# Kernel optimization log

Measured on AMD Instinct MI355X. Metric: run time of the kernel, lower is better.

## Reference

```python
import jax, jax.numpy as jnp
import numpy as np

NUM_USERS = 100000
NUM_ITEMS = 50000
EMBED_DIM = 64
N_NODES = NUM_USERS + NUM_ITEMS
N_EDGES = 4800000
N_LAYERS = 3


def setup_inputs() -> dict:
    key = jax.random.key(0)
    k = jax.random.split(key, 7)
    return {
        "users": jax.random.randint(k[0], (16384,), 0, NUM_USERS),
        "items": jax.random.randint(k[1], (16384,), 0, NUM_ITEMS),
        "user_emb": jax.random.normal(k[2], (NUM_USERS, EMBED_DIM), dtype=jnp.float32) * 0.1,
        "item_emb": jax.random.normal(k[3], (NUM_ITEMS, EMBED_DIM), dtype=jnp.float32) * 0.1,
        "adj_rows": jax.random.randint(k[4], (N_EDGES,), 0, N_NODES),
        "adj_cols": jax.random.randint(k[5], (N_EDGES,), 0, N_NODES),
        "adj_vals": jax.random.uniform(k[6], (N_EDGES,), dtype=jnp.float32) * (1.0 / 32.0),
    }


def _spmm(rows, cols, vals, x):
    # y[r] = sum_{e: rows[e]==r} vals[e] * x[cols[e]]   (COO SpMM)
    msgs = vals[:, None] * x[cols]              # [nnz, d]
    return jax.ops.segment_sum(msgs, rows, num_segments=N_NODES)


def reference(users, items, user_emb, item_emb, adj_rows, adj_cols, adj_vals):
    ego = jnp.concatenate([user_emb, item_emb], axis=0)   # [N, d]
    acc = ego                                             # running sum of layer outputs
    h = ego
    for _ in range(N_LAYERS):
        h = _spmm(adj_rows, adj_cols, adj_vals, h)
        acc = acc + h
    final = acc / jnp.asarray(N_LAYERS + 1, dtype=acc.dtype)  # mean over layers
    final_users = final[:NUM_USERS]
    final_items = final[NUM_USERS:]
    u = final_users[users]                                # [B, d]
    v = final_items[items]                                # [B, d]
    return jnp.sum(u * v, axis=1)                         # [B]
```

## Files before the change

kernel.cpp:

```cpp
#include <hip/hip_runtime.h>

#define NUM_USERS 100000
#define NUM_ITEMS 50000
#define EMBED_DIM 64
#define N_NODES   (NUM_USERS + NUM_ITEMS)
#define N_EDGES   4800000
#define N_QUERY   16384

#define NODE_FLOATS ((size_t)N_NODES * EMBED_DIM)
#define NODE_FLOAT4 (NODE_FLOATS / 4)

#define NBUCKET    256
#define BROWS      586
#define BUCKET_CAP 20480
#define BIN_EDGES  8192
#define BIN_THREADS 512
#define BIN_BLOCKS ((N_EDGES + BIN_EDGES - 1) / BIN_EDGES)

__device__ __forceinline__ float4 bf2f4(uint2 u) {
    float4 f;
    f.x = __uint_as_float(u.x << 16);
    f.y = __uint_as_float(u.x & 0xFFFF0000u);
    f.z = __uint_as_float(u.y << 16);
    f.w = __uint_as_float(u.y & 0xFFFF0000u);
    return f;
}
__device__ __forceinline__ unsigned rne_bf(float f) {
    unsigned b = __float_as_uint(f);
    return (b + 0x7FFFu + ((b >> 16) & 1u)) >> 16;
}
__device__ __forceinline__ uint2 f42bf(float4 f) {
    uint2 u;
    u.x = rne_bf(f.x) | (rne_bf(f.y) << 16);
    u.y = rne_bf(f.z) | (rne_bf(f.w) << 16);
    return u;
}
__device__ __forceinline__ void fma4v(float v, float4 xv, float4& av) {
    av.x = fmaf(v, xv.x, av.x);
    av.y = fmaf(v, xv.y, av.y);
    av.z = fmaf(v, xv.z, av.z);
    av.w = fmaf(v, xv.w, av.w);
}

__global__ void init_gcur_kernel(int* __restrict__ gcur) {
    if (threadIdx.x < NBUCKET)
        gcur[threadIdx.x] = threadIdx.x * BUCKET_CAP;
}

__global__ void ego_bf_kernel(const float4* __restrict__ ue4,
                              const float4* __restrict__ ie4,
                              uint2* __restrict__ ego) {
    size_t i = (size_t)blockIdx.x * blockDim.x + threadIdx.x;
    if (i >= NODE_FLOAT4) return;
    const size_t user_f4 = (size_t)NUM_USERS * EMBED_DIM / 4;
    float4 v = (i < user_f4) ? ue4[i] : ie4[i - user_f4];
    ego[i] = f42bf(v);
}

__global__ void __launch_bounds__(BIN_THREADS) bin_kernel(
        const int* __restrict__ rows,
        const int* __restrict__ cols,
        const float* __restrict__ vals,
        int* __restrict__ gcur,
        int2* __restrict__ rec) {
    __shared__ int  lcnt[NBUCKET];
    __shared__ int  lbase[NBUCKET];
    __shared__ int  loff[NBUCKET];
    __shared__ int  lcur[NBUCKET];
    __shared__ int  scan[NBUCKET];
    __shared__ int2 sRec[BIN_EDGES];

    const int tid = threadIdx.x;
    if (tid < NBUCKET) lcnt[tid] = 0;
    __syncthreads();

    const size_t e0 = (size_t)blockIdx.x * BIN_EDGES;

    for (int k = tid; k < BIN_EDGES; k += BIN_THREADS) {
        size_t e = e0 + k;
        if (e < N_EDGES)
            atomicAdd(&lcnt[rows[e] / BROWS], 1);
    }
    __syncthreads();

    if (tid < NBUCKET) {
        lbase[tid] = atomicAdd(&gcur[tid], lcnt[tid]);
        scan[tid]  = lcnt[tid];
    }
    __syncthreads();
    for (int off = 1; off < NBUCKET; off <<= 1) {
        int tv = (tid < NBUCKET && tid >= off) ? scan[tid - off] : 0;
        __syncthreads();
        if (tid < NBUCKET) scan[tid] += tv;
        __syncthreads();
    }
    if (tid < NBUCKET) {
        loff[tid] = scan[tid] - lcnt[tid];
        lcur[tid] = loff[tid];
    }
    __syncthreads();

    for (int k = tid; k < BIN_EDGES; k += BIN_THREADS) {
        size_t e = e0 + k;
        if (e < N_EDGES) {
            int r  = rows[e];
            int b  = r / BROWS;
            int rl = r - b * BROWS;
            int slot = atomicAdd(&lcur[b], 1);
            sRec[slot] = make_int2((rl << 18) | cols[e], __float_as_int(vals[e]));
        }
    }
    __syncthreads();

    int wv = tid >> 6, ln = tid & 63;
    for (int b = wv; b < NBUCKET; b += (BIN_THREADS / 64)) {
        int n = lcnt[b], src = loff[b], dst = lbase[b];
        for (int k = ln; k < n; k += 64)
            rec[(size_t)dst + k] = sRec[src + k];
    }
}

__global__ void __launch_bounds__(256) csr_kernel(
        const int2* __restrict__ rec,
        const int* __restrict__ gcur,
        int* __restrict__ row_start,
        int* __restrict__ row_cnt,
        int2* __restrict__ pair) {
    __shared__ int hist[BROWS + 2];
    __shared__ int excl[768];
    __shared__ int part[256];

    const int b    = blockIdx.x;
    const int base = b * BUCKET_CAP;
    const int n    = gcur[b] - base;
    const int lo   = b * BROWS;
    const int t    = threadIdx.x;

    for (int j = t; j < BROWS; j += 256) hist[j] = 0;
    __syncthreads();

    for (int i = t; i < n; i += 256)
        atomicAdd(&hist[rec[base + i].x >> 18], 1);
    __syncthreads();

    int vloc[3];
    int s0 = 0;
    #pragma unroll
    for (int k = 0; k < 3; ++k) {
        int idx = t * 3 + k;
        int v = (idx < BROWS) ? ((hist[idx] + 1) & ~1) : 0;
        vloc[k] = s0;
        s0 += v;
    }
    part[t] = s0;
    __syncthreads();
    for (int off = 1; off < 256; off <<= 1) {
        int tv = (t >= off) ? part[t - off] : 0;
        __syncthreads();
        part[t] += tv;
        __syncthreads();
    }
    int pbase = part[t] - s0;
    #pragma unroll
    for (int k = 0; k < 3; ++k) {
        int idx = t * 3 + k;
        if (idx < BROWS) excl[idx] = pbase + vloc[k];
    }
    __syncthreads();

    for (int j = t; j < BROWS; j += 256) {
        row_start[lo + j] = base + excl[j];
        row_cnt[lo + j]   = hist[j];
    }
    __syncthreads();

    for (int i = t; i < n; i += 256) {
        int2 p = rec[base + i];
        int rl = p.x >> 18;
        int slot = atomicAdd(&excl[rl], 1);
        pair[(size_t)base + slot] = make_int2(p.x & 0x3FFFF, p.y);
    }
}

__device__ __forceinline__ float4 gather_row(int s, int e, int g, int q,
                                             const int2* __restrict__ pair,
                                             const uint2* __restrict__ hb) {
    float4 av = make_float4(0.f, 0.f, 0.f, 0.f);
    int i = s;
    for (; i + 32 <= e; i += 32) {
        int4 pp0 = *(const int4*)(pair + i      + 2*g);
        int4 pp1 = *(const int4*)(pair + i +  8 + 2*g);
        int4 pp2 = *(const int4*)(pair + i + 16 + 2*g);
        int4 pp3 = *(const int4*)(pair + i + 24 + 2*g);
        uint2 u0 = hb[(size_t)pp0.x * 16 + q];
        uint2 u1 = hb[(size_t)pp0.z * 16 + q];
        uint2 u2 = hb[(size_t)pp1.x * 16 + q];
        uint2 u3 = hb[(size_t)pp1.z * 16 + q];
        uint2 u4 = hb[(size_t)pp2.x * 16 + q];
        uint2 u5 = hb[(size_t)pp2.z * 16 + q];
        uint2 u6 = hb[(size_t)pp3.x * 16 + q];
        uint2 u7 = hb[(size_t)pp3.z * 16 + q];
        fma4v(__int_as_float(pp0.y), bf2f4(u0), av);
        fma4v(__int_as_float(pp0.w), bf2f4(u1), av);
        fma4v(__int_as_float(pp1.y), bf2f4(u2), av);
        fma4v(__int_as_float(pp1.w), bf2f4(u3), av);
        fma4v(__int_as_float(pp2.y), bf2f4(u4), av);
        fma4v(__int_as_float(pp2.w), bf2f4(u5), av);
        fma4v(__int_as_float(pp3.y), bf2f4(u6), av);
        fma4v(__int_as_float(pp3.w), bf2f4(u7), av);
    }
    if (i + 16 <= e) {
        int4 pp0 = *(const int4*)(pair + i     + 2*g);
        int4 pp1 = *(const int4*)(pair + i + 8 + 2*g);
        uint2 u0 = hb[(size_t)pp0.x * 16 + q];
        uint2 u1 = hb[(size_t)pp0.z * 16 + q];
        uint2 u2 = hb[(size_t)pp1.x * 16 + q];
        uint2 u3 = hb[(size_t)pp1.z * 16 + q];
        fma4v(__int_as_float(pp0.y), bf2f4(u0), av);
        fma4v(__int_as_float(pp0.w), bf2f4(u1), av);
        fma4v(__int_as_float(pp1.y), bf2f4(u2), av);
        fma4v(__int_as_float(pp1.w), bf2f4(u3), av);
        i += 16;
    }
    if (i + 8 <= e) {
        int4 pp0 = *(const int4*)(pair + i + 2*g);
        uint2 u0 = hb[(size_t)pp0.x * 16 + q];
        uint2 u1 = hb[(size_t)pp0.z * 16 + q];
        fma4v(__int_as_float(pp0.y), bf2f4(u0), av);
        fma4v(__int_as_float(pp0.w), bf2f4(u1), av);
        i += 8;
    }
    if (i + 4 <= e) {
        int2 p0 = pair[i + g];
        uint2 u0 = hb[(size_t)p0.x * 16 + q];
        fma4v(__int_as_float(p0.y), bf2f4(u0), av);
        i += 4;
    }
    if (i < e) {
        int idx = i + g;
        int2 pD = pair[(idx < e) ? idx : (e - 1)];
        float vD = (idx < e) ? __int_as_float(pD.y) : 0.0f;
        uint2 uD = hb[(size_t)pD.x * 16 + q];
        fma4v(vD, bf2f4(uD), av);
    }
    av.x += __shfl_xor(av.x, 32, 64);
    av.y += __shfl_xor(av.y, 32, 64);
    av.z += __shfl_xor(av.z, 32, 64);
    av.w += __shfl_xor(av.w, 32, 64);
    av.x += __shfl_xor(av.x, 16, 64);
    av.y += __shfl_xor(av.y, 16, 64);
    av.z += __shfl_xor(av.z, 16, 64);
    av.w += __shfl_xor(av.w, 16, 64);
    return av;
}

__global__ void spmm_kernel(const int* __restrict__ row_start,
                            const int* __restrict__ row_cnt,
                            const int2* __restrict__ pair,
                            const uint2* __restrict__ hb,
                            uint2* __restrict__ hn) {
    int wid  = (int)(((size_t)blockIdx.x * blockDim.x + threadIdx.x) >> 6);
    int lane = threadIdx.x & 63;
    int g = lane >> 4, q = lane & 15;
    if (wid >= N_NODES) return;
    int s = row_start[wid];
    int e = s + row_cnt[wid];

    float4 av = gather_row(s, e, g, q, pair, hb);

    if (lane < 16)
        hn[(size_t)wid * 16 + q] = f42bf(av);
}

__global__ void final_kernel(const int* __restrict__ row_start,
                             const int* __restrict__ row_cnt,
                             const int2* __restrict__ pair,
                             const uint2* __restrict__ hB,
                             const uint2* __restrict__ hA,
                             const float4* __restrict__ ue4,
                             const float4* __restrict__ ie4,
                             float4* __restrict__ fin4,
                             const int* __restrict__ users,
                             const int* __restrict__ items) {
    int wid  = (int)(((size_t)blockIdx.x * blockDim.x + threadIdx.x) >> 6);
    int lane = threadIdx.x & 63;
    int g = lane >> 4, q = lane & 15;
    if (wid >= 2 * N_QUERY) return;
    int row = (wid < N_QUERY) ? users[wid] : (NUM_USERS + items[wid - N_QUERY]);
    int s = row_start[row];
    int e = s + row_cnt[row];

    float4 av = gather_row(s, e, g, q, pair, hB);

    if (lane < 16) {
        size_t o = (size_t)row * 16 + q;
        float4 ego = (row < NUM_USERS)
                   ? ue4[(size_t)row * 16 + q]
                   : ie4[(size_t)(row - NUM_USERS) * 16 + q];
        float4 a1 = bf2f4(hA[o]);
        float4 a2 = bf2f4(hB[o]);
        float4 f;
        f.x = 0.25f * (ego.x + a1.x + a2.x + av.x);
        f.y = 0.25f * (ego.y + a1.y + a2.y + av.y);
        f.z = 0.25f * (ego.z + a1.z + a2.z + av.z);
        f.w = 0.25f * (ego.w + a1.w + a2.w + av.w);
        fin4[o] = f;
    }
}

__global__ void dot_kernel(const int* __restrict__ users,
                           const int* __restrict__ items,
                           const float* __restrict__ fin,
                           float* __restrict__ out) {
    int lane = threadIdx.x & 63;
    int wave = threadIdx.x >> 6;
    int q    = blockIdx.x * (blockDim.x >> 6) + wave;
    if (q >= N_QUERY) return;

    float a = fin[(size_t)users[q] * EMBED_DIM + lane];
    float b = fin[((size_t)NUM_USERS + items[q]) * EMBED_DIM + lane];
    float p = a * b;

    #pragma unroll
    for (int off = 32; off >= 1; off >>= 1)
        p += __shfl_xor(p, off, 64);

    if (lane == 0)
        out[q] = p;
}

extern "C" void kernel_launch(void* const* d_in, const int* in_sizes, int n_in,
                              void* d_out, int out_size, void* d_ws, size_t ws_size,
                              hipStream_t stream) {
    const int*   users = (const int*)  d_in[0];
    const int*   items = (const int*)  d_in[1];
    const float* ue    = (const float*)d_in[2];
    const float* ie    = (const float*)d_in[3];
    const int*   rows  = (const int*)  d_in[4];
    const int*   cols  = (const int*)  d_in[5];
    const float* vals  = (const float*)d_in[6];
    float*       out   = (float*)d_out;

    const size_t REC_N = (size_t)NBUCKET * BUCKET_CAP;

    float* fin    = (float*)d_ws;
    uint2* ego_bf = (uint2*)(fin + NODE_FLOATS);
    uint2* hA_bf  = ego_bf + NODE_FLOAT4;
    uint2* hB_bf  = hA_bf + NODE_FLOAT4;
    int2*  rec    = (int2*)ego_bf;
    int2*  pair   = (int2*)(hB_bf + NODE_FLOAT4);

    int* row_start = (int*)(pair + REC_N);
    int* row_cnt   = row_start + 150016;
    int* gcur      = row_cnt + 150016;

    int vec_blocks = (int)((NODE_FLOAT4 + 255) / 256);

    init_gcur_kernel<<<1, 256, 0, stream>>>(gcur);
    bin_kernel<<<BIN_BLOCKS, BIN_THREADS, 0, stream>>>(rows, cols, vals, gcur, rec);
    csr_kernel<<<NBUCKET, 256, 0, stream>>>(rec, gcur, row_start, row_cnt, pair);

    ego_bf_kernel<<<vec_blocks, 256, 0, stream>>>(
        (const float4*)ue, (const float4*)ie, ego_bf);

    int spmm_blocks = (N_NODES * 64 + 255) / 256;
    spmm_kernel<<<spmm_blocks, 256, 0, stream>>>(row_start, row_cnt, pair, ego_bf, hA_bf);
    spmm_kernel<<<spmm_blocks, 256, 0, stream>>>(row_start, row_cnt, pair, hA_bf, hB_bf);

    int q_blocks = (2 * N_QUERY * 64 + 255) / 256;
    final_kernel<<<q_blocks, 256, 0, stream>>>(row_start, row_cnt, pair,
        hB_bf, hA_bf, (const float4*)ue, (const float4*)ie, (float4*)fin,
        users, items);

    dot_kernel<<<(N_QUERY + 3) / 4, 256, 0, stream>>>(users, items, fin, out);
}
```

Baseline: 335.6 us.

## Fuse ego conversion into CSR build, merge final and dot into score kernel

```diff
diff --git a/kernel.cpp b/kernel.cpp
--- a/kernel.cpp
+++ b/kernel.cpp
@@ -16,6 +16,7 @@
 #define BIN_EDGES  8192
 #define BIN_THREADS 512
 #define BIN_BLOCKS ((N_EDGES + BIN_EDGES - 1) / BIN_EDGES)
+#define EGO_SLICE  (NODE_FLOAT4 / NBUCKET)
 
 __device__ __forceinline__ float4 bf2f4(uint2 u) {
     float4 f;
@@ -40,21 +41,6 @@
     av.y = fmaf(v, xv.y, av.y);
     av.z = fmaf(v, xv.z, av.z);
     av.w = fmaf(v, xv.w, av.w);
-}
-
-__global__ void init_gcur_kernel(int* __restrict__ gcur) {
-    if (threadIdx.x < NBUCKET)
-        gcur[threadIdx.x] = threadIdx.x * BUCKET_CAP;
-}
-
-__global__ void ego_bf_kernel(const float4* __restrict__ ue4,
-                              const float4* __restrict__ ie4,
-                              uint2* __restrict__ ego) {
-    size_t i = (size_t)blockIdx.x * blockDim.x + threadIdx.x;
-    if (i >= NODE_FLOAT4) return;
-    const size_t user_f4 = (size_t)NUM_USERS * EMBED_DIM / 4;
-    float4 v = (i < user_f4) ? ue4[i] : ie4[i - user_f4];
-    ego[i] = f42bf(v);
 }
 
 __global__ void __launch_bounds__(BIN_THREADS) bin_kernel(
@@ -69,22 +55,22 @@
     __shared__ int  lcur[NBUCKET];
     __shared__ int  scan[NBUCKET];
     __shared__ int2 sRec[BIN_EDGES];
+    __shared__ unsigned char sBkt[BIN_EDGES];
 
     const int tid = threadIdx.x;
     if (tid < NBUCKET) lcnt[tid] = 0;
     __syncthreads();
 
     const size_t e0 = (size_t)blockIdx.x * BIN_EDGES;
-
-    for (int k = tid; k < BIN_EDGES; k += BIN_THREADS) {
-        size_t e = e0 + k;
-        if (e < N_EDGES)
-            atomicAdd(&lcnt[rows[e] / BROWS], 1);
-    }
+    const int nrec = (int)(((size_t)N_EDGES - e0) < BIN_EDGES ? (N_EDGES - e0)
+                                                              : BIN_EDGES);
+
+    for (int k = tid; k < nrec; k += BIN_THREADS)
+        atomicAdd(&lcnt[rows[e0 + k] / BROWS], 1);
     __syncthreads();
 
     if (tid < NBUCKET) {
-        lbase[tid] = atomicAdd(&gcur[tid], lcnt[tid]);
+        lbase[tid] = tid * BUCKET_CAP + atomicAdd(&gcur[tid], lcnt[tid]);
         scan[tid]  = lcnt[tid];
     }
     __syncthreads();
@@ -100,23 +86,20 @@
     }
     __syncthreads();
 
-    for (int k = tid; k < BIN_EDGES; k += BIN_THREADS) {
-        size_t e = e0 + k;
-        if (e < N_EDGES) {
-            int r  = rows[e];
-            int b  = r / BROWS;
-            int rl = r - b * BROWS;
-            int slot = atomicAdd(&lcur[b], 1);
-            sRec[slot] = make_int2((rl << 18) | cols[e], __float_as_int(vals[e]));
-        }
-    }
-    __syncthreads();
-
-    int wv = tid >> 6, ln = tid & 63;
-    for (int b = wv; b < NBUCKET; b += (BIN_THREADS / 64)) {
-        int n = lcnt[b], src = loff[b], dst = lbase[b];
-        for (int k = ln; k < n; k += 64)
-            rec[(size_t)dst + k] = sRec[src + k];
+    for (int k = tid; k < nrec; k += BIN_THREADS) {
+        int r  = rows[e0 + k];
+        int b  = r / BROWS;
+        int rl = r - b * BROWS;
+        int slot = atomicAdd(&lcur[b], 1);
+        sRec[slot] = make_int2((rl << 18) | cols[e0 + k],
+                               __float_as_int(vals[e0 + k]));
+        sBkt[slot] = (unsigned char)b;
+    }
+    __syncthreads();
+
+    for (int k = tid; k < nrec; k += BIN_THREADS) {
+        int bk = sBkt[k];
+        rec[(size_t)lbase[bk] + (k - loff[bk])] = sRec[k];
     }
 }
 
@@ -125,16 +108,29 @@
         const int* __restrict__ gcur,
         int* __restrict__ row_start,
         int* __restrict__ row_cnt,
-        int2* __restrict__ pair) {
+        int2* __restrict__ pair,
+        const float4* __restrict__ ue4,
+        const float4* __restrict__ ie4,
+        uint2* __restrict__ ego) {
     __shared__ int hist[BROWS + 2];
     __shared__ int excl[768];
     __shared__ int part[256];
 
     const int b    = blockIdx.x;
     const int base = b * BUCKET_CAP;
-    const int n    = gcur[b] - base;
+    const int n    = gcur[b];
     const int lo   = b * BROWS;
     const int t    = threadIdx.x;
+
+    {
+        const size_t user_f4 = (size_t)NUM_USERS * EMBED_DIM / 4;
+        size_t s0 = (size_t)b * EGO_SLICE;
+        for (int j = t; j < EGO_SLICE; j += 256) {
+            size_t idx = s0 + j;
+            float4 v = (idx < user_f4) ? ue4[idx] : ie4[idx - user_f4];
+            ego[idx] = f42bf(v);
+        }
+    }
 
     for (int j = t; j < BROWS; j += 256) hist[j] = 0;
     __syncthreads();
@@ -272,26 +268,18 @@
         hn[(size_t)wid * 16 + q] = f42bf(av);
 }
 
-__global__ void final_kernel(const int* __restrict__ row_start,
-                             const int* __restrict__ row_cnt,
-                             const int2* __restrict__ pair,
-                             const uint2* __restrict__ hB,
-                             const uint2* __restrict__ hA,
-                             const float4* __restrict__ ue4,
-                             const float4* __restrict__ ie4,
-                             float4* __restrict__ fin4,
-                             const int* __restrict__ users,
-                             const int* __restrict__ items) {
-    int wid  = (int)(((size_t)blockIdx.x * blockDim.x + threadIdx.x) >> 6);
-    int lane = threadIdx.x & 63;
-    int g = lane >> 4, q = lane & 15;
-    if (wid >= 2 * N_QUERY) return;
-    int row = (wid < N_QUERY) ? users[wid] : (NUM_USERS + items[wid - N_QUERY]);
+__device__ __forceinline__ float4 fin_row(int row, int g, int q, int lane,
+                                          const int* __restrict__ row_start,
+                                          const int* __restrict__ row_cnt,
+                                          const int2* __restrict__ pair,
+                                          const uint2* __restrict__ hA,
+                                          const uint2* __restrict__ hB,
+                                          const float4* __restrict__ ue4,
+                                          const float4* __restrict__ ie4) {
     int s = row_start[row];
     int e = s + row_cnt[row];
-
     float4 av = gather_row(s, e, g, q, pair, hB);
-
+    float4 f = make_float4(0.f, 0.f, 0.f, 0.f);
     if (lane < 16) {
         size_t o = (size_t)row * 16 + q;
         float4 ego = (row < NUM_USERS)
@@ -299,34 +287,43 @@
                    : ie4[(size_t)(row - NUM_USERS) * 16 + q];
         float4 a1 = bf2f4(hA[o]);
         float4 a2 = bf2f4(hB[o]);
-        float4 f;
         f.x = 0.25f * (ego.x + a1.x + a2.x + av.x);
         f.y = 0.25f * (ego.y + a1.y + a2.y + av.y);
         f.z = 0.25f * (ego.z + a1.z + a2.z + av.z);
         f.w = 0.25f * (ego.w + a1.w + a2.w + av.w);
-        fin4[o] = f;
-    }
-}
-
-__global__ void dot_kernel(const int* __restrict__ users,
-                           const int* __restrict__ items,
-                           const float* __restrict__ fin,
-                           float* __restrict__ out) {
+    }
+    return f;
+}
+
+__global__ void score_kernel(const int* __restrict__ row_start,
+                             const int* __restrict__ row_cnt,
+                             const int2* __restrict__ pair,
+                             const uint2* __restrict__ hA,
+                             const uint2* __restrict__ hB,
+                             const float4* __restrict__ ue4,
+                             const float4* __restrict__ ie4,
+                             const int* __restrict__ users,
+                             const int* __restrict__ items,
+                             float* __restrict__ out) {
+    int qid  = (int)(((size_t)blockIdx.x * blockDim.x + threadIdx.x) >> 6);
     int lane = threadIdx.x & 63;
-    int wave = threadIdx.x >> 6;
-    int q    = blockIdx.x * (blockDim.x >> 6) + wave;
-    if (q >= N_QUERY) return;
-
-    float a = fin[(size_t)users[q] * EMBED_DIM + lane];
-    float b = fin[((size_t)NUM_USERS + items[q]) * EMBED_DIM + lane];
-    float p = a * b;
-
-    #pragma unroll
-    for (int off = 32; off >= 1; off >>= 1)
-        p += __shfl_xor(p, off, 64);
+    int g = lane >> 4, q = lane & 15;
+    if (qid >= N_QUERY) return;
+
+    int urow = users[qid];
+    int irow = NUM_USERS + items[qid];
+
+    float4 fu = fin_row(urow, g, q, lane, row_start, row_cnt, pair, hA, hB, ue4, ie4);
+    float4 fi = fin_row(irow, g, q, lane, row_start, row_cnt, pair, hA, hB, ue4, ie4);
+
+    float p = fu.x * fi.x + fu.y * fi.y + fu.z * fi.z + fu.w * fi.w;
+    p += __shfl_xor(p, 8, 64);
+    p += __shfl_xor(p, 4, 64);
+    p += __shfl_xor(p, 2, 64);
+    p += __shfl_xor(p, 1, 64);
 
     if (lane == 0)
-        out[q] = p;
+        out[qid] = p;
 }
 
 extern "C" void kernel_launch(void* const* d_in, const int* in_sizes, int n_in,
@@ -343,34 +340,27 @@
 
     const size_t REC_N = (size_t)NBUCKET * BUCKET_CAP;
 
-    float* fin    = (float*)d_ws;
-    uint2* ego_bf = (uint2*)(fin + NODE_FLOATS);
+    uint2* ego_bf = (uint2*)d_ws;
     uint2* hA_bf  = ego_bf + NODE_FLOAT4;
     uint2* hB_bf  = hA_bf + NODE_FLOAT4;
-    int2*  rec    = (int2*)ego_bf;
-    int2*  pair   = (int2*)(hB_bf + NODE_FLOAT4);
+    int2*  rec    = (int2*)(hB_bf + NODE_FLOAT4);
+    int2*  pair   = rec + REC_N;
 
     int* row_start = (int*)(pair + REC_N);
     int* row_cnt   = row_start + 150016;
     int* gcur      = row_cnt + 150016;
 
-    int vec_blocks = (int)((NODE_FLOAT4 + 255) / 256);
-
-    init_gcur_kernel<<<1, 256, 0, stream>>>(gcur);
+    (void)hipMemsetAsync(gcur, 0, NBUCKET * sizeof(int), stream);
+
     bin_kernel<<<BIN_BLOCKS, BIN_THREADS, 0, stream>>>(rows, cols, vals, gcur, rec);
-    csr_kernel<<<NBUCKET, 256, 0, stream>>>(rec, gcur, row_start, row_cnt, pair);
-
-    ego_bf_kernel<<<vec_blocks, 256, 0, stream>>>(
+    csr_kernel<<<NBUCKET, 256, 0, stream>>>(rec, gcur, row_start, row_cnt, pair,
         (const float4*)ue, (const float4*)ie, ego_bf);
 
     int spmm_blocks = (N_NODES * 64 + 255) / 256;
     spmm_kernel<<<spmm_blocks, 256, 0, stream>>>(row_start, row_cnt, pair, ego_bf, hA_bf);
     spmm_kernel<<<spmm_blocks, 256, 0, stream>>>(row_start, row_cnt, pair, hA_bf, hB_bf);
 
-    int q_blocks = (2 * N_QUERY * 64 + 255) / 256;
-    final_kernel<<<q_blocks, 256, 0, stream>>>(row_start, row_cnt, pair,
-        hB_bf, hA_bf, (const float4*)ue, (const float4*)ie, (float4*)fin,
-        users, items);
-
-    dot_kernel<<<(N_QUERY + 3) / 4, 256, 0, stream>>>(users, items, fin, out);
-}
+    int score_blocks = (N_QUERY * 64 + 255) / 256;
+    score_kernel<<<score_blocks, 256, 0, stream>>>(row_start, row_cnt, pair,
+        hA_bf, hB_bf, (const float4*)ue, (const float4*)ie, users, items, out);
+}
```

Measured after the change: 333.6 us. Within noise of the previous version (-0.6%).
